# Kernel optimization log

Hardware: AMD Instinct MI355X
Metric: run time of the kernel (lower is better)

## Reference

```python
import jax, jax.numpy as jnp
import numpy as np

EPS_RMS = 1e-4   # RunningMeanStd epsilon (mean=0, var=1 at init)
LN_EPS = 1e-5    # torch LayerNorm default
NUM_HEADS = 16


def _layernorm(x, g, b):
    m = x.mean(-1, keepdims=True)
    v = ((x - m) ** 2).mean(-1, keepdims=True)
    return (x - m) / jnp.sqrt(v + LN_EPS) * g + b


def _rms_normalize(a):
    # RunningMeanStd.normalize with mean=0, var=1: clip(a / sqrt(1+eps), -5, 5)
    return jnp.clip(a / jnp.sqrt(1.0 + EPS_RMS), -5.0, 5.0)


def _sinusoidal_pe(pos, d):
    # pos [...,] -> [..., d]; matches torch code: div_term over arange(d//2)
    div = jnp.exp(jnp.arange(d // 2, dtype=jnp.float32) * (-np.log(1000.0) / d))
    ang = pos[..., None] * div                         # [..., d//2]
    pe = jnp.zeros(pos.shape + (d,), dtype=jnp.float32)
    pe = pe.at[..., 0::2].set(jnp.sin(ang))
    pe = pe.at[..., 1::2].set(jnp.cos(ang))
    return pe


def _encoder_layer(xs, mask, Wqkv, bqkv, Wo, bo, g1, be1, g2, be2, Wf1, bf1, Wf2, bf2):
    # post-LN TransformerEncoderLayer with boolean attention mask [B,S,S]
    B, S, D = xs.shape
    hd = D // NUM_HEADS
    qkv = xs @ Wqkv.T + bqkv                           # [B,S,3D]
    q, k, v = jnp.split(qkv, 3, axis=-1)
    q = q.reshape(B, S, NUM_HEADS, hd).transpose(0, 2, 1, 3)
    k = k.reshape(B, S, NUM_HEADS, hd).transpose(0, 2, 1, 3)
    v = v.reshape(B, S, NUM_HEADS, hd).transpose(0, 2, 1, 3)
    scores = jnp.einsum('bhqd,bhkd->bhqk', q, k) / jnp.sqrt(jnp.float32(hd))
    scores = jnp.where(mask[:, None, :, :], -jnp.inf, scores)
    attn = jax.nn.softmax(scores, axis=-1)
    o = jnp.einsum('bhqk,bhkd->bhqd', attn, v).transpose(0, 2, 1, 3).reshape(B, S, D)
    o = o @ Wo.T + bo
    xs = _layernorm(xs + o, g1, be1)
    ff = jax.nn.gelu(xs @ Wf1.T + bf1, approximate=False) @ Wf2.T + bf2
    xs = _layernorm(xs + ff, g2, be2)
    return xs


def reference(x, w, y, W_nail, b_nail, W_cond, b_cond, Wqkv, bqkv, Wo, bo,
              ln1_g, ln1_b, ln2_g, ln2_b, W1, b1, W2, b2, W_ham, b_ham):
    B, Lx = x.shape[0], x.shape[1]
    n_w = w.shape[1] * w.shape[2]
    L = Lx + n_w + 1                                   # total_paragraph_length
    S = L - 1
    D = W_nail.shape[0]

    w_last = w[:, -1]                                  # [B, P, 6]

    # embed_x
    t = jnp.nan_to_num(x[..., 0])
    xc = jnp.nan_to_num(x)
    xx = _rms_normalize(xc)[..., 1:] @ W_nail.T + b_nail   # [B,Lx,D]
    xx = xx + _sinusoidal_pe(t, D)
    x_mask = jnp.isnan(x[..., 0])                      # [B,Lx]

    # embed_w
    wc = jnp.nan_to_num(w)
    wn = _rms_normalize(wc).reshape(B, -1, w.shape[-1])    # [B,Lw*P,6]
    ww = wn @ W_cond.T + b_cond                        # [B,Lw*P,D]

    tgt = jnp.concatenate([xx, ww], axis=1)            # [B,S,D]

    # custom per-batch boolean mask: causal, but columns [0,Lx) follow x padding mask
    causal = jnp.triu(jnp.ones((S, S), dtype=bool), 1)
    mask = jnp.broadcast_to(causal, (B, S, S))
    mask = mask.at[:, :, :Lx].set(x_mask[:, None, :])

    # global positional encoding added only on the w-token segment
    pe_g = _sinusoidal_pe(jnp.arange(L, dtype=jnp.float32), D)  # [L,D]
    tgt = tgt.at[:, Lx:].add(pe_g[Lx:L - 1])

    for i in range(Wqkv.shape[0]):
        tgt = _encoder_layer(tgt, mask, Wqkv[i], bqkv[i], Wo[i], bo[i],
                             ln1_g[i], ln1_b[i], ln2_g[i], ln2_b[i],
                             W1[i], b1[i], W2[i], b2[i])

    y_resid_hat = (tgt[:, -1] @ W_ham.T + b_ham).reshape(B, -1, 6)
    y_resid = jax.lax.stop_gradient(y - w_last)
    loss = jnp.mean((y_resid_hat - y_resid) ** 2)
    return loss


def setup_inputs() -> dict:
    key = jax.random.key(0)
    ks = jax.random.split(key, 16)
    NL, D, FF, HAM = 4, 1024, 4096, 144
    s = 0.02
    return {
        'x': jax.random.normal(ks[0], (8, 512, 64), jnp.float32),
        'w': jax.random.normal(ks[1], (8, 16, 24, 6), jnp.float32),
        'y': jax.random.normal(ks[2], (8, 24, 6), jnp.float32),
        'W_nail': jax.random.normal(ks[3], (D, 63), jnp.float32) * s,
        'b_nail': jnp.zeros((D,), jnp.float32),
        'W_cond': jax.random.normal(ks[4], (D, 6), jnp.float32) * s,
        'b_cond': jnp.zeros((D,), jnp.float32),
        'Wqkv': jax.random.normal(ks[5], (NL, 3 * D, D), jnp.float32) * s,
        'bqkv': jnp.zeros((NL, 3 * D), jnp.float32),
        'Wo': jax.random.normal(ks[6], (NL, D, D), jnp.float32) * s,
        'bo': jnp.zeros((NL, D), jnp.float32),
        'ln1_g': jnp.ones((NL, D), jnp.float32),
        'ln1_b': jnp.zeros((NL, D), jnp.float32),
        'ln2_g': jnp.ones((NL, D), jnp.float32),
        'ln2_b': jnp.zeros((NL, D), jnp.float32),
        'W1': jax.random.normal(ks[7], (NL, FF, D), jnp.float32) * s,
        'b1': jnp.zeros((NL, FF), jnp.float32),
        'W2': jax.random.normal(ks[8], (NL, D, FF), jnp.float32) * s,
        'b2': jnp.zeros((NL, D), jnp.float32),
        'W_ham': jax.random.normal(ks[9], (HAM, D), jnp.float32) * s,
        'b_ham': jnp.zeros((HAM,), jnp.float32),
    }
```

## Files before the change

### kernel.cpp

```cpp
#include <hip/hip_runtime.h>
#include <math.h>


#define B_      8
#define LX_     512
#define NW_     384
#define S_      896
#define D_      1024
#define H_      16
#define HD_     64
#define FF_     4096
#define HAM_    144

#define RMS_SCALE 0.9999500037496876f
#define PE_C     (-6.907755278982137f / 1024.0f)

typedef __bf16 bf16x4 __attribute__((ext_vector_type(4)));
typedef __bf16 bf16x8 __attribute__((ext_vector_type(8)));
typedef float  f32x4  __attribute__((ext_vector_type(4)));

static __device__ __forceinline__ float nan0(float v) { return (v != v) ? 0.0f : v; }

static __device__ __forceinline__ void async_copy16(const __bf16* g, __bf16* l) {
    __builtin_amdgcn_global_load_lds(
        (const __attribute__((address_space(1))) void*)g,
        (__attribute__((address_space(3))) void*)l, 16, 0, 0);
}

static __device__ __forceinline__ float fast_gelu(float x) {
    float x3 = x * x * x;
    float z = 0.7978845608028654f * x + 0.035677408136300125f * x3;
    float az = fabsf(z);
    float e = __expf(2.0f * az);
    float t = 1.0f - 2.0f / (e + 1.0f);
    t = (z < 0.0f) ? -t : t;
    return 0.5f * x * (1.0f + t);
}

__global__ __launch_bounds__(256) void convert4_kernel(
        const float* __restrict__ s0, const float* __restrict__ s1,
        const float* __restrict__ s2, const float* __restrict__ s3,
        __bf16* __restrict__ d0, __bf16* __restrict__ d1,
        __bf16* __restrict__ d2, __bf16* __restrict__ d3) {
    int blk = blockIdx.x;
    const float* src; __bf16* dst; int base;
    if (blk < 3072)      { src = s0; dst = d0; base = blk; }
    else if (blk < 4096) { src = s1; dst = d1; base = blk - 3072; }
    else if (blk < 8192) { src = s2; dst = d2; base = blk - 4096; }
    else                 { src = s3; dst = d3; base = blk - 8192; }
    int i = (base * 256 + threadIdx.x) * 4;
    float4 v = *(const float4*)&src[i];
    bf16x4 o = {(__bf16)v.x, (__bf16)v.y, (__bf16)v.z, (__bf16)v.w};
    *(bf16x4*)&dst[i] = o;
}

__global__ __launch_bounds__(256) void transpose_nail_kernel(
        const float* __restrict__ W_nail, float* __restrict__ WT) {
    int i = blockIdx.x * 256 + threadIdx.x;
    int d = i & 1023, kk = i >> 10;
    WT[kk * 1024 + d] = W_nail[d * 63 + kk];
}

__global__ __launch_bounds__(256) void embed_x_kernel(
        const float* __restrict__ x, const float* __restrict__ WT,
        const float* __restrict__ b_nail, __bf16* __restrict__ tgt_bf,
        int* __restrict__ xmask) {
    int row0 = blockIdx.x * 8;
    int tid = threadIdx.x;
    __shared__ float xn[8][64];
    __shared__ float ts[8];
#pragma unroll
    for (int it = 0; it < 2; ++it) {
        int i = tid + it * 256;
        int r = i >> 6, c = i & 63;
        float vv = x[(size_t)(row0 + r) * 64 + c];
        float v0 = nan0(vv);
        xn[r][c] = fminf(fmaxf(v0 * RMS_SCALE, -5.0f), 5.0f);
        if (c == 0) { ts[r] = v0; xmask[row0 + r] = (vv != vv) ? 1 : 0; }
    }
    __syncthreads();
    int d0 = tid * 4;
    float4 bz = *(const float4*)&b_nail[d0];
    float acc[8][4];
#pragma unroll
    for (int r = 0; r < 8; ++r) {
        acc[r][0] = bz.x; acc[r][1] = bz.y; acc[r][2] = bz.z; acc[r][3] = bz.w;
    }
    for (int k = 0; k < 63; ++k) {
        float4 wv = *(const float4*)&WT[k * 1024 + d0];
#pragma unroll
        for (int r = 0; r < 8; ++r) {
            float xv = xn[r][k + 1];
            acc[r][0] += xv * wv.x; acc[r][1] += xv * wv.y;
            acc[r][2] += xv * wv.z; acc[r][3] += xv * wv.w;
        }
    }
    float div[4];
#pragma unroll
    for (int j = 0; j < 4; ++j)
        div[j] = __expf((float)((d0 + j) >> 1) * PE_C);
#pragma unroll
    for (int r = 0; r < 8; ++r) {
        int row = row0 + r;
        int b = row >> 9, i = row & 511;
        float t = ts[r];
        bf16x4 ob;
#pragma unroll
        for (int j = 0; j < 4; ++j) {
            float ang = t * div[j];
            float pe = ((d0 + j) & 1) ? __cosf(ang) : __sinf(ang);
            ob[j] = (__bf16)(acc[r][j] + pe);
        }
        *(bf16x4*)&tgt_bf[((size_t)b * S_ + i) * D_ + d0] = ob;
    }
}

__global__ __launch_bounds__(256) void embed_w_kernel(
        const float* __restrict__ w, const float* __restrict__ W_cond,
        const float* __restrict__ b_cond, __bf16* __restrict__ tgt_bf) {
    int row = blockIdx.x;
    int b = row / NW_, j = row % NW_;
    const float* wr = w + (long)row * 6;
    float wn[6];
#pragma unroll
    for (int k = 0; k < 6; ++k)
        wn[k] = fminf(fmaxf(nan0(wr[k]) * RMS_SCALE, -5.0f), 5.0f);
    int tid = threadIdx.x;
    int d0 = tid * 4;
    float pos = (float)(LX_ + j);
    bf16x4 ob;
#pragma unroll
    for (int jj = 0; jj < 4; ++jj) {
        int d = d0 + jj;
        float acc = b_cond[d];
        const float* wc = W_cond + (long)d * 6;
#pragma unroll
        for (int k = 0; k < 6; ++k) acc += wn[k] * wc[k];
        float dv = expf((float)(d >> 1) * PE_C);
        float ang = pos * dv;
        ob[jj] = (__bf16)(acc + ((d & 1) ? cosf(ang) : sinf(ang)));
    }
    *(bf16x4*)&tgt_bf[((long)b * S_ + LX_ + j) * D_ + d0] = ob;
}


#define LDA(BUF, MH) do {                                                      \
    _Pragma("unroll")                                                          \
    for (int i_ = 0; i_ < 4; ++i_) {                                           \
        const int row_ = (MH) * 128 + wr * 64 + i_ * 16 + frow;                \
        _Pragma("unroll")                                                      \
        for (int k_ = 0; k_ < 2; ++k_)                                         \
            a[i_][k_] = *(const bf16x8*)&As[BUF][row_ * 64 +                   \
                (((quad + k_ * 4) ^ sf) * 8)];                                 \
    }                                                                          \
} while (0)

#define LDB(BUF, NH) do {                                                      \
    _Pragma("unroll")                                                          \
    for (int j_ = 0; j_ < NJ; ++j_) {                                          \
        const int row_ = (BN == 256)                                           \
            ? ((NH) * 128 + j_ * 16 + wc * 32 + frow)                          \
            : ((NH) * 64 + wc * 16 + frow);                                    \
        _Pragma("unroll")                                                      \
        for (int k_ = 0; k_ < 2; ++k_)                                         \
            b[(NH) * NJ + j_][k_] = *(const bf16x8*)&Bs[BUF][row_ * 64 +       \
                (((quad + k_ * 4) ^ sf) * 8)];                                 \
    }                                                                          \
} while (0)

#define MMA(MH, NH) do {                                                       \
    _Pragma("unroll")                                                          \
    for (int i_ = 0; i_ < 4; ++i_)                                             \
        _Pragma("unroll")                                                      \
        for (int j_ = 0; j_ < NJ; ++j_)                                        \
            _Pragma("unroll")                                                  \
            for (int k_ = 0; k_ < 2; ++k_)                                     \
                acc[(MH) * 4 + i_][(NH) * NJ + j_] =                           \
                    __builtin_amdgcn_mfma_f32_16x16x32_bf16(                   \
                        b[(NH) * NJ + j_][k_], a[i_][k_],                      \
                        acc[(MH) * 4 + i_][(NH) * NJ + j_], 0, 0, 0);          \
} while (0)

#define STAGE_A(BUF, H, KT) do {                                               \
    const __bf16* g_ = Ag + (size_t)((H) * 128) * K + ((size_t)(KT) << 6);     \
    async_copy16(g_, &As[BUF][((H) * 128) * 64 + dst8]);                       \
    async_copy16(g_ + ((size_t)K << 6), &As[BUF][((H) * 128 + 64) * 64 + dst8]); \
} while (0)

#define STAGE_B(BUF, H, KT) do {                                               \
    if constexpr (BN == 256) {                                                 \
        const __bf16* g_ = Wg + (size_t)((H) * 128) * K + ((size_t)(KT) << 6); \
        async_copy16(g_, &Bs[BUF][((H) * 128) * 64 + dst8]);                   \
        async_copy16(g_ + ((size_t)K << 6),                                    \
                     &Bs[BUF][((H) * 128 + 64) * 64 + dst8]);                  \
    } else {                                                                   \
        const __bf16* g_ = Wg + (size_t)((H) * 64) * K + ((size_t)(KT) << 6);  \
        async_copy16(g_, &Bs[BUF][((H) * 64) * 64 + dst8]);                    \
    }                                                                          \
} while (0)

#define PHASE_SYNC() do {                                                      \
    __builtin_amdgcn_sched_barrier(0);                                         \
    __builtin_amdgcn_s_barrier();                                              \
    asm volatile("s_waitcnt lgkmcnt(0)" ::: "memory");                         \
    __builtin_amdgcn_sched_barrier(0);                                         \
} while (0)

#define PHASE_END() do {                                                       \
    __builtin_amdgcn_sched_barrier(0);                                         \
    __builtin_amdgcn_s_barrier();                                              \
} while (0)

#define VM_MAIN do {                                                           \
    if constexpr (BN == 256) { asm volatile("s_waitcnt vmcnt(6)" ::: "memory"); } \
    else                     { asm volatile("s_waitcnt vmcnt(4)" ::: "memory"); } \
} while (0)
#define VM_ZERO asm volatile("s_waitcnt vmcnt(0)" ::: "memory")
#define VM_NONE ((void)0)

#define GTILE(S1, S2, VMOP) do {                                               \
    const int bf_ = t & 1;                                                     \
                          \
    LDA(bf_, 0); LDB(bf_, 0);                                                  \
    if (S1) STAGE_A(bf_ ^ 1, 1, t + 1);                                        \
    PHASE_SYNC();                                                              \
    __builtin_amdgcn_s_setprio(1); MMA(0, 0); __builtin_amdgcn_s_setprio(0);   \
    PHASE_END();                                                               \
                    \
    LDB(bf_, 1);                                                               \
    if (S2) STAGE_B(bf_, 0, t + 2);                                            \
    PHASE_SYNC();                                                              \
    __builtin_amdgcn_s_setprio(1); MMA(0, 1); __builtin_amdgcn_s_setprio(0);   \
    PHASE_END();                                                               \
                                     \
    LDA(bf_, 1);                                                               \
    if (S2) STAGE_A(bf_, 0, t + 2);                                            \
    PHASE_SYNC();                                                              \
    __builtin_amdgcn_s_setprio(1); MMA(1, 0); __builtin_amdgcn_s_setprio(0);   \
    PHASE_END();                                                               \
            \
    if (S2) STAGE_B(bf_, 1, t + 2);                                            \
    VMOP;                                                                      \
    PHASE_SYNC();                                                              \
    __builtin_amdgcn_s_setprio(1); MMA(1, 1); __builtin_amdgcn_s_setprio(0);   \
    PHASE_END();                                                               \
} while (0)

template <int BN, int MODE>
__global__ __launch_bounds__(512, 2) void gemm8p(
        const __bf16* __restrict__ A, const __bf16* __restrict__ W,
        const float* __restrict__ bias,
        __bf16* __restrict__ Cb,
        __bf16* __restrict__ Cq, __bf16* __restrict__ Ck, __bf16* __restrict__ Cv,
        int M, int N, int K) {
    constexpr int NI = BN / 64;
    constexpr int NJ = NI / 2;
    static_assert(BN == 256 || BN == 128, "BN");
    __shared__ __attribute__((aligned(16))) __bf16 As[2][256 * 64];
    __shared__ __attribute__((aligned(16))) __bf16 Bs[2][BN * 64];

    const int tid = threadIdx.x;
    const int wave = tid >> 6, lane = tid & 63;
    const int wr = wave >> 2, wc = wave & 3;
    const int frow = lane & 15, quad = lane >> 4;
    const int sf = frow & 7;
    const int m0 = blockIdx.y * 256, n0 = blockIdx.x * BN;

    const int sr = tid >> 3;
    const int scol = ((tid & 7) ^ (sr & 7)) * 8;
    const __bf16* Ag = A + (size_t)(m0 + sr) * K + scol;
    const __bf16* Wg = W + (size_t)(n0 + sr) * K + scol;
    const int dst8 = tid * 8;

    f32x4 acc[8][NI];
#pragma unroll
    for (int i = 0; i < 8; ++i)
#pragma unroll
        for (int j = 0; j < NI; ++j) acc[i][j] = 0.0f;
    bf16x8 a[4][2];
    bf16x8 b[NI][2];

    const int NT = K >> 6;

    STAGE_B(0, 0, 0); STAGE_A(0, 0, 0); STAGE_B(0, 1, 0); STAGE_A(0, 1, 0);
    STAGE_B(1, 0, 1); STAGE_A(1, 0, 1); STAGE_B(1, 1, 1);
    VM_MAIN;
    __builtin_amdgcn_s_barrier();

    int t = 0;
    for (; t < NT - 2; ++t) { GTILE(1, 1, VM_MAIN); }
    GTILE(1, 0, VM_ZERO);
    ++t;
    GTILE(0, 0, VM_NONE);

#pragma unroll
    for (int ni = 0; ni < NI; ++ni) {
        int cg0;
        if constexpr (BN == 256)
            cg0 = n0 + (ni >> 1) * 128 + (ni & 1) * 16 + wc * 32 + quad * 4;
        else
            cg0 = n0 + ni * 64 + wc * 16 + quad * 4;
        float4 bv = *(const float4*)&bias[cg0];
        float bz[4] = {bv.x, bv.y, bv.z, bv.w};
#pragma unroll
        for (int mi = 0; mi < 8; ++mi) {
            int rg = m0 + (mi >> 2) * 128 + wr * 64 + (mi & 3) * 16 + frow;
            float vv[4];
#pragma unroll
            for (int r = 0; r < 4; ++r) {
                float v = acc[mi][ni][r] + bz[r];
                if (MODE == 1) v = fast_gelu(v);
                vv[r] = v;
            }
            bf16x4 o = {(__bf16)vv[0], (__bf16)vv[1], (__bf16)vv[2], (__bf16)vv[3]};
            if (MODE == 2) {
                int which = cg0 >> 10;
                int h = (cg0 & 1023) >> 6;
                int e = cg0 & 63;
                int bb = rg / S_, s = rg % S_;
                __bf16* dstp = (which == 0) ? Cq : (which == 1) ? Ck : Cv;
                *(bf16x4*)&dstp[(((size_t)bb * H_ + h) * S_ + s) * HD_ + e] = o;
            } else {
                *(bf16x4*)&Cb[(size_t)rg * N + cg0] = o;
            }
        }
    }
}

__global__ __launch_bounds__(256) void attn_mfma(
        const __bf16* __restrict__ q, const __bf16* __restrict__ k,
        const __bf16* __restrict__ v, const int* __restrict__ xmask,
        __bf16* __restrict__ ctx) {
    __shared__ __bf16 Ks[64][72];
    __shared__ __bf16 Vt[64][66];
    __shared__ __bf16 Ps[4][16][72];
    __shared__ float mb[LX_];
    int tid = threadIdx.x;
    int wave = tid >> 6, lane = tid & 63;
    int frow = lane & 15, quad = lane >> 4;
    int blk = blockIdx.x;
    int qt = blk % 14;
    int bh = blk / 14;
    int b = bh >> 4, h = bh & 15;
    int q0 = qt * 64;
    int q0w = q0 + wave * 16;
    size_t base = (size_t)bh * S_ * HD_;

    for (int i = tid; i < LX_; i += 256)
        mb[i] = xmask[(b << 9) + i] ? -INFINITY : 0.0f;

    const __bf16* qrow = q + base + (size_t)(q0w + frow) * HD_ + quad * 8;
    bf16x8 aq0 = *(const bf16x8*)qrow;
    bf16x8 aq1 = *(const bf16x8*)(qrow + 32);

    f32x4 o[4];
#pragma unroll
    for (int dt = 0; dt < 4; ++dt) o[dt] = 0.0f;
    float mrow[4] = {-INFINITY, -INFINITY, -INFINITY, -INFINITY};
    float lrow[4] = {0.0f, 0.0f, 0.0f, 0.0f};

    int kend = (q0 >= LX_) ? (q0 + 64) : LX_;

    int sr = tid >> 2;
    int sc = (tid & 3) * 8;
    const __bf16* kg = k + base + (size_t)sr * HD_ + sc;
    const __bf16* vg = v + base + (size_t)sr * HD_ + sc;

    for (int k0 = 0; k0 < kend; k0 += 64) {
        {
            size_t off = (size_t)k0 * HD_;
            bf16x8 k0v = *(const bf16x8*)(kg + off);
            bf16x8 k1v = *(const bf16x8*)(kg + off + 32);
            *(bf16x8*)&Ks[sr][sc] = k0v;
            *(bf16x8*)&Ks[sr][sc + 32] = k1v;
            bf16x8 v0v = *(const bf16x8*)(vg + off);
            bf16x8 v1v = *(const bf16x8*)(vg + off + 32);
#pragma unroll
            for (int j = 0; j < 8; ++j) {
                Vt[sc + j][sr] = v0v[j];
                Vt[sc + 32 + j][sr] = v1v[j];
            }
        }
        __syncthreads();

        f32x4 scr[4];
#pragma unroll
        for (int nt = 0; nt < 4; ++nt) {
            bf16x8 bk0 = *(const bf16x8*)&Ks[nt * 16 + frow][quad * 8];
            bf16x8 bk1 = *(const bf16x8*)&Ks[nt * 16 + frow][32 + quad * 8];
            f32x4 z = 0.0f;
            z = __builtin_amdgcn_mfma_f32_16x16x32_bf16(aq0, bk0, z, 0, 0, 0);
            z = __builtin_amdgcn_mfma_f32_16x16x32_bf16(aq1, bk1, z, 0, 0, 0);
            scr[nt] = z;
        }

        float tmax[4] = {-INFINITY, -INFINITY, -INFINITY, -INFINITY};
#pragma unroll
        for (int nt = 0; nt < 4; ++nt) {
            int kj = k0 + nt * 16 + frow;
            float bias = (kj < LX_) ? mb[kj] : 0.0f;
#pragma unroll
            for (int r = 0; r < 4; ++r) {
                float s = scr[nt][r] * 0.125f + bias;
                if (kj >= LX_ && kj > q0w + quad * 4 + r) s = -INFINITY;
                scr[nt][r] = s;
                tmax[r] = fmaxf(tmax[r], s);
            }
        }
#pragma unroll
        for (int off = 1; off < 16; off <<= 1)
#pragma unroll
            for (int r = 0; r < 4; ++r)
                tmax[r] = fmaxf(tmax[r], __shfl_xor(tmax[r], off, 64));

        float alpha[4], rsum[4];
#pragma unroll
        for (int r = 0; r < 4; ++r) {
            float nm = fmaxf(mrow[r], tmax[r]);
            alpha[r] = (nm == -INFINITY) ? 1.0f : __expf(mrow[r] - nm);
            mrow[r] = nm;
            rsum[r] = 0.0f;
        }
#pragma unroll
        for (int nt = 0; nt < 4; ++nt) {
#pragma unroll
            for (int r = 0; r < 4; ++r) {
                float s = scr[nt][r];
                float p = (s == -INFINITY) ? 0.0f : __expf(s - mrow[r]);
                rsum[r] += p;
                Ps[wave][quad * 4 + r][nt * 16 + frow] = (__bf16)p;
            }
        }
#pragma unroll
        for (int off = 1; off < 16; off <<= 1)
#pragma unroll
            for (int r = 0; r < 4; ++r)
                rsum[r] += __shfl_xor(rsum[r], off, 64);
#pragma unroll
        for (int r = 0; r < 4; ++r)
            lrow[r] = lrow[r] * alpha[r] + rsum[r];
#pragma unroll
        for (int dt = 0; dt < 4; ++dt)
#pragma unroll
            for (int r = 0; r < 4; ++r)
                o[dt][r] *= alpha[r];

        bf16x8 ap0 = *(const bf16x8*)&Ps[wave][frow][quad * 8];
        bf16x8 ap1 = *(const bf16x8*)&Ps[wave][frow][32 + quad * 8];
#pragma unroll
        for (int dt = 0; dt < 4; ++dt) {
            bf16x8 bv0 = *(const bf16x8*)&Vt[dt * 16 + frow][quad * 8];
            bf16x8 bv1 = *(const bf16x8*)&Vt[dt * 16 + frow][32 + quad * 8];
            o[dt] = __builtin_amdgcn_mfma_f32_16x16x32_bf16(ap0, bv0, o[dt], 0, 0, 0);
            o[dt] = __builtin_amdgcn_mfma_f32_16x16x32_bf16(ap1, bv1, o[dt], 0, 0, 0);
        }
        __syncthreads();
    }

#pragma unroll
    for (int r = 0; r < 4; ++r) {
        float inv = (lrow[r] > 0.0f) ? 1.0f / lrow[r] : 0.0f;
        int qg = q0w + quad * 4 + r;
        size_t ob = ((size_t)b * S_ + qg) * D_ + h * HD_;
#pragma unroll
        for (int dt = 0; dt < 4; ++dt)
            ctx[ob + dt * 16 + frow] = (__bf16)(o[dt][r] * inv);
    }
}

__global__ __launch_bounds__(256) void add_ln_kernel(
        __bf16* __restrict__ xs_bf, const __bf16* __restrict__ o,
        const float* __restrict__ g, const float* __restrict__ bb) {
    long row = blockIdx.x;
    __bf16* xr = xs_bf + row * D_;
    const __bf16* orr = o + row * D_;
    int tid = threadIdx.x;
    bf16x4 a4 = *(const bf16x4*)&xr[tid * 4];
    bf16x4 b4v = *(const bf16x4*)&orr[tid * 4];
    float vv[4];
#pragma unroll
    for (int j = 0; j < 4; ++j) vv[j] = (float)a4[j] + (float)b4v[j];
    float s = vv[0] + vv[1] + vv[2] + vv[3];
    __shared__ float red[4];
    __shared__ float stat;
#pragma unroll
    for (int off = 32; off; off >>= 1) s += __shfl_down(s, off, 64);
    if ((tid & 63) == 0) red[tid >> 6] = s;
    __syncthreads();
    if (tid == 0) stat = (red[0] + red[1] + red[2] + red[3]) * (1.0f / 1024.0f);
    __syncthreads();
    float mean = stat;
    float d[4];
    float s2 = 0.0f;
#pragma unroll
    for (int j = 0; j < 4; ++j) { d[j] = vv[j] - mean; s2 += d[j] * d[j]; }
    __syncthreads();
#pragma unroll
    for (int off = 32; off; off >>= 1) s2 += __shfl_down(s2, off, 64);
    if ((tid & 63) == 0) red[tid >> 6] = s2;
    __syncthreads();
    if (tid == 0) stat = (red[0] + red[1] + red[2] + red[3]) * (1.0f / 1024.0f);
    __syncthreads();
    float inv = 1.0f / sqrtf(stat + 1e-5f);
    float4 gg = *(const float4*)&g[tid * 4];
    float4 bv = *(const float4*)&bb[tid * 4];
    float g4[4] = {gg.x, gg.y, gg.z, gg.w};
    float b4[4] = {bv.x, bv.y, bv.z, bv.w};
    bf16x4 ob;
#pragma unroll
    for (int j = 0; j < 4; ++j) ob[j] = (__bf16)(d[j] * inv * g4[j] + b4[j]);
    *(bf16x4*)&xr[tid * 4] = ob;
}

__global__ __launch_bounds__(256) void head_kernel(
        const __bf16* __restrict__ tgt_bf, const float* __restrict__ W_ham,
        const float* __restrict__ b_ham, float* __restrict__ out) {
    int b = blockIdx.x;
    int tid = threadIdx.x;
    __shared__ float xr[D_];
    const __bf16* row = tgt_bf + ((long)b * S_ + (S_ - 1)) * D_;
    for (int i = tid; i < D_; i += 256) xr[i] = (float)row[i];
    __syncthreads();
    for (int n = tid; n < HAM_; n += 256) {
        float acc = b_ham[n];
        const float* wr = W_ham + (long)n * D_;
        for (int kk = 0; kk < D_; ++kk) acc += xr[kk] * wr[kk];
        out[b * HAM_ + n] = acc;
    }
}

__global__ __launch_bounds__(256) void loss_kernel(
        const float* __restrict__ head_out, const float* __restrict__ y,
        const float* __restrict__ w, float* __restrict__ out) {
    int tid = threadIdx.x;
    float acc = 0.0f;
    for (int i = tid; i < B_ * HAM_; i += 256) {
        int b = i / HAM_, r = i % HAM_;
        float w_last = w[((long)b * 16 + 15) * HAM_ + r];
        float resid = y[i] - w_last;
        float dd = head_out[i] - resid;
        acc += dd * dd;
    }
    __shared__ float red[4];
#pragma unroll
    for (int off = 32; off; off >>= 1) acc += __shfl_down(acc, off, 64);
    if ((tid & 63) == 0) red[tid >> 6] = acc;
    __syncthreads();
    if (tid == 0)
        out[0] = (red[0] + red[1] + red[2] + red[3]) * (1.0f / (B_ * HAM_));
}

extern "C" void kernel_launch(void* const* d_in, const int* in_sizes, int n_in,
                              void* d_out, int out_size, void* d_ws, size_t ws_size,
                              hipStream_t stream) {
    const float* x      = (const float*)d_in[0];
    const float* w      = (const float*)d_in[1];
    const float* y      = (const float*)d_in[2];
    const float* W_nail = (const float*)d_in[3];
    const float* b_nail = (const float*)d_in[4];
    const float* W_cond = (const float*)d_in[5];
    const float* b_cond = (const float*)d_in[6];
    const float* Wqkv   = (const float*)d_in[7];
    const float* bqkv   = (const float*)d_in[8];
    const float* Wo     = (const float*)d_in[9];
    const float* bo     = (const float*)d_in[10];
    const float* ln1_g  = (const float*)d_in[11];
    const float* ln1_b  = (const float*)d_in[12];
    const float* ln2_g  = (const float*)d_in[13];
    const float* ln2_b  = (const float*)d_in[14];
    const float* W1     = (const float*)d_in[15];
    const float* b1     = (const float*)d_in[16];
    const float* W2     = (const float*)d_in[17];
    const float* b2     = (const float*)d_in[18];
    const float* W_ham  = (const float*)d_in[19];
    const float* b_ham  = (const float*)d_in[20];

    float* ws = (float*)d_ws;
    const long SEG = (long)B_ * S_ * D_;
    float*  W_nailT = ws;
    __bf16* tmp_bf = (__bf16*)(ws + SEG);
    __bf16* tgt_bf = (__bf16*)(ws + 2 * SEG);
    __bf16* ctx_bf = (__bf16*)(ws + 2 * SEG + SEG / 2);
    __bf16* qb     = (__bf16*)(ws + 3 * SEG);
    __bf16* kb     = (__bf16*)(ws + 3 * SEG + SEG / 2);
    __bf16* vb     = (__bf16*)(ws + 4 * SEG);
    __bf16* ffh_bf = (__bf16*)(ws + 2 * SEG + SEG / 2);
    __bf16* wbf    = (__bf16*)(ws + 4 * SEG + SEG / 2);
    int*    xmask    = (int*)(ws + 4 * SEG + SEG / 2 + 6291456);
    float*  head_out = ws + 4 * SEG + SEG / 2 + 6291456 + 4096;

    __bf16* wqkv_bf = wbf;
    __bf16* wo_bf   = wbf + 3145728;
    __bf16* w1_bf   = wbf + 4194304;
    __bf16* w2_bf   = wbf + 8388608;

    const int M = B_ * S_;

    transpose_nail_kernel<<<252, 256, 0, stream>>>(W_nail, W_nailT);
    embed_x_kernel<<<B_ * LX_ / 8, 256, 0, stream>>>(x, W_nailT, b_nail, tgt_bf, xmask);
    embed_w_kernel<<<B_ * NW_, 256, 0, stream>>>(w, W_cond, b_cond, tgt_bf);

    for (int L = 0; L < 4; ++L) {
        const int NQ = 3 * D_ * D_, NO = D_ * D_, N1 = FF_ * D_, N2 = D_ * FF_;
        convert4_kernel<<<12288, 256, 0, stream>>>(
            Wqkv + (size_t)L * NQ, Wo + (size_t)L * NO,
            W1 + (size_t)L * N1, W2 + (size_t)L * N2,
            wqkv_bf, wo_bf, w1_bf, w2_bf);

        gemm8p<256, 2><<<dim3(3 * D_ / 256, M / 256), 512, 0, stream>>>(
            tgt_bf, wqkv_bf, bqkv + (size_t)L * 3 * D_,
            nullptr, qb, kb, vb, M, 3 * D_, D_);
        attn_mfma<<<B_ * H_ * (S_ / 64), 256, 0, stream>>>(qb, kb, vb, xmask, ctx_bf);
        gemm8p<128, 0><<<dim3(D_ / 128, M / 256), 512, 0, stream>>>(
            ctx_bf, wo_bf, bo + (size_t)L * D_,
            tmp_bf, nullptr, nullptr, nullptr, M, D_, D_);
        add_ln_kernel<<<M, 256, 0, stream>>>(tgt_bf, tmp_bf,
            ln1_g + (size_t)L * D_, ln1_b + (size_t)L * D_);
        gemm8p<256, 1><<<dim3(FF_ / 256, M / 256), 512, 0, stream>>>(
            tgt_bf, w1_bf, b1 + (size_t)L * FF_,
            ffh_bf, nullptr, nullptr, nullptr, M, FF_, D_);
        gemm8p<128, 0><<<dim3(D_ / 128, M / 256), 512, 0, stream>>>(
            ffh_bf, w2_bf, b2 + (size_t)L * D_,
            tmp_bf, nullptr, nullptr, nullptr, M, D_, FF_);
        add_ln_kernel<<<M, 256, 0, stream>>>(tgt_bf, tmp_bf,
            ln2_g + (size_t)L * D_, ln2_b + (size_t)L * D_);
    }

    head_kernel<<<B_, 256, 0, stream>>>(tgt_bf, W_ham, b_ham, head_out);
    loss_kernel<<<1, 256, 0, stream>>>(head_out, y, w, (float*)d_out);
}
```

Before: 1.874 ms.

## Store V transposed from QKV GEMM and double-buffer attention K/V with async LDS loads

The QKV GEMM epilogue now writes V in a [b,h,d,s] transposed layout, so attention can stream K and V tiles straight into XOR-swizzled LDS with async global-to-LDS copies. The tiles are double-buffered, with the next one prefetched while the current one is computed, and MFMA sections get raised priority. The out-projection GEMM switches to a simpler 128x128 kernel with 256 threads. Attention blocks are also remapped so that the blocks for one (b,h) land on the same XCD. The trade-off is that the transposed V writes become scalar scattered stores in the QKV epilogue.

```diff
diff --git a/kernel.cpp b/kernel.cpp
--- a/kernel.cpp
+++ b/kernel.cpp
@@ -220,25 +220,21 @@
 
 #define GTILE(S1, S2, VMOP) do {                                               \
     const int bf_ = t & 1;                                                     \
-                          \
     LDA(bf_, 0); LDB(bf_, 0);                                                  \
     if (S1) STAGE_A(bf_ ^ 1, 1, t + 1);                                        \
     PHASE_SYNC();                                                              \
     __builtin_amdgcn_s_setprio(1); MMA(0, 0); __builtin_amdgcn_s_setprio(0);   \
     PHASE_END();                                                               \
-                    \
     LDB(bf_, 1);                                                               \
     if (S2) STAGE_B(bf_, 0, t + 2);                                            \
     PHASE_SYNC();                                                              \
     __builtin_amdgcn_s_setprio(1); MMA(0, 1); __builtin_amdgcn_s_setprio(0);   \
     PHASE_END();                                                               \
-                                     \
     LDA(bf_, 1);                                                               \
     if (S2) STAGE_A(bf_, 0, t + 2);                                            \
     PHASE_SYNC();                                                              \
     __builtin_amdgcn_s_setprio(1); MMA(1, 0); __builtin_amdgcn_s_setprio(0);   \
     PHASE_END();                                                               \
-            \
     if (S2) STAGE_B(bf_, 1, t + 2);                                            \
     VMOP;                                                                      \
     PHASE_SYNC();                                                              \
@@ -312,39 +308,137 @@
                 if (MODE == 1) v = fast_gelu(v);
                 vv[r] = v;
             }
-            bf16x4 o = {(__bf16)vv[0], (__bf16)vv[1], (__bf16)vv[2], (__bf16)vv[3]};
             if (MODE == 2) {
                 int which = cg0 >> 10;
                 int h = (cg0 & 1023) >> 6;
                 int e = cg0 & 63;
                 int bb = rg / S_, s = rg % S_;
-                __bf16* dstp = (which == 0) ? Cq : (which == 1) ? Ck : Cv;
-                *(bf16x4*)&dstp[(((size_t)bb * H_ + h) * S_ + s) * HD_ + e] = o;
+                if (which == 2) {
+                    size_t vb = ((size_t)bb * H_ + h) * HD_ + e;
+#pragma unroll
+                    for (int r = 0; r < 4; ++r)
+                        Cv[(vb + r) * S_ + s] = (__bf16)vv[r];
+                } else {
+                    bf16x4 o = {(__bf16)vv[0], (__bf16)vv[1], (__bf16)vv[2], (__bf16)vv[3]};
+                    __bf16* dstp = (which == 0) ? Cq : Ck;
+                    *(bf16x4*)&dstp[(((size_t)bb * H_ + h) * S_ + s) * HD_ + e] = o;
+                }
             } else {
+                bf16x4 o = {(__bf16)vv[0], (__bf16)vv[1], (__bf16)vv[2], (__bf16)vv[3]};
                 *(bf16x4*)&Cb[(size_t)rg * N + cg0] = o;
             }
         }
     }
 }
 
+template <int MODE>
+__global__ __launch_bounds__(256) void gemm_mfma(
+        const __bf16* __restrict__ A, const __bf16* __restrict__ W,
+        const float* __restrict__ bias,
+        __bf16* __restrict__ Cb,
+        int M, int N, int K) {
+    __shared__ __bf16 As[128 * 64];
+    __shared__ __bf16 Bs[128 * 64];
+    int tid = threadIdx.x;
+    int wave = tid >> 6, lane = tid & 63;
+    int m0 = blockIdx.y * 128, n0 = blockIdx.x * 128;
+    int wm = (wave >> 1) * 64, wn = (wave & 1) * 64;
+
+    int srow = wave * 32 + (lane >> 3);
+    int scol = ((lane & 7) ^ (lane >> 3)) * 8;
+    const __bf16* Ag = A + (size_t)(m0 + srow) * K + scol;
+    const __bf16* Wg = W + (size_t)(n0 + srow) * K + scol;
+    __bf16* Al = &As[wave * 2048];
+    __bf16* Bl = &Bs[wave * 2048];
+
+    f32x4 acc[4][4];
+#pragma unroll
+    for (int i = 0; i < 4; ++i)
+#pragma unroll
+        for (int j = 0; j < 4; ++j) acc[i][j] = 0.0f;
+
+    int frow = lane & 15;
+    int quad = lane >> 4;
+    int sf = frow & 7;
+
+    for (int k0 = 0; k0 < K; k0 += 64) {
+        size_t off = (size_t)k0;
+        async_copy16(Ag + off,                  Al);
+        async_copy16(Ag + off + (size_t)8 * K,  Al + 512);
+        async_copy16(Ag + off + (size_t)16 * K, Al + 1024);
+        async_copy16(Ag + off + (size_t)24 * K, Al + 1536);
+        async_copy16(Wg + off,                  Bl);
+        async_copy16(Wg + off + (size_t)8 * K,  Bl + 512);
+        async_copy16(Wg + off + (size_t)16 * K, Bl + 1024);
+        async_copy16(Wg + off + (size_t)24 * K, Bl + 1536);
+        __syncthreads();
+#pragma unroll
+        for (int ks = 0; ks < 2; ++ks) {
+            int slot = ((quad + ks * 4) ^ sf) * 8;
+            bf16x8 a[4], b[4];
+#pragma unroll
+            for (int mi = 0; mi < 4; ++mi)
+                a[mi] = *(const bf16x8*)&As[(wm + mi * 16 + frow) * 64 + slot];
+#pragma unroll
+            for (int ni = 0; ni < 4; ++ni)
+                b[ni] = *(const bf16x8*)&Bs[(wn + ni * 16 + frow) * 64 + slot];
+#pragma unroll
+            for (int mi = 0; mi < 4; ++mi)
+#pragma unroll
+                for (int ni = 0; ni < 4; ++ni)
+                    acc[mi][ni] = __builtin_amdgcn_mfma_f32_16x16x32_bf16(
+                        b[ni], a[mi], acc[mi][ni], 0, 0, 0);
+        }
+        __syncthreads();
+    }
+
+    int mrow_l = lane & 15;
+    int nq = (lane >> 4) * 4;
+#pragma unroll
+    for (int ni = 0; ni < 4; ++ni) {
+        int cg0 = n0 + wn + ni * 16 + nq;
+        float4 bv = *(const float4*)&bias[cg0];
+        float bz[4] = {bv.x, bv.y, bv.z, bv.w};
+#pragma unroll
+        for (int mi = 0; mi < 4; ++mi) {
+            int rg = m0 + wm + mi * 16 + mrow_l;
+            float vv[4];
+#pragma unroll
+            for (int r = 0; r < 4; ++r) {
+                float v = acc[mi][ni][r] + bz[r];
+                if (MODE == 1) v = fast_gelu(v);
+                vv[r] = v;
+            }
+            bf16x4 o = {(__bf16)vv[0], (__bf16)vv[1], (__bf16)vv[2], (__bf16)vv[3]};
+            *(bf16x4*)&Cb[(size_t)rg * N + cg0] = o;
+        }
+    }
+}
+
 __global__ __launch_bounds__(256) void attn_mfma(
         const __bf16* __restrict__ q, const __bf16* __restrict__ k,
-        const __bf16* __restrict__ v, const int* __restrict__ xmask,
+        const __bf16* __restrict__ vt, const int* __restrict__ xmask,
         __bf16* __restrict__ ctx) {
-    __shared__ __bf16 Ks[64][72];
-    __shared__ __bf16 Vt[64][66];
-    __shared__ __bf16 Ps[4][16][72];
+    __shared__ __attribute__((aligned(16))) __bf16 Ks[2][64 * 64];
+    __shared__ __attribute__((aligned(16))) __bf16 Vs[2][64 * 64];
+    __shared__ __attribute__((aligned(16))) __bf16 Ps[4][16 * 64];
     __shared__ float mb[LX_];
     int tid = threadIdx.x;
     int wave = tid >> 6, lane = tid & 63;
     int frow = lane & 15, quad = lane >> 4;
+    int f7 = frow & 7, f3 = frow >> 3;
+    int sl0 = (quad ^ f7) * 8;
+    int sl1 = ((quad + 4) ^ f7) * 8;
+
     int blk = blockIdx.x;
-    int qt = blk % 14;
-    int bh = blk / 14;
+    int xcd = blk & 7, slot = blk >> 3;
+    int bh = xcd * 16 + slot / 14;
+    int qt = slot % 14;
     int b = bh >> 4, h = bh & 15;
     int q0 = qt * 64;
     int q0w = q0 + wave * 16;
     size_t base = (size_t)bh * S_ * HD_;
+    size_t vbase = (size_t)bh * HD_ * S_;
 
     for (int i = tid; i < LX_; i += 256)
         mb[i] = xmask[(b << 9) + i] ? -INFINITY : 0.0f;
@@ -360,39 +454,50 @@
     float lrow[4] = {0.0f, 0.0f, 0.0f, 0.0f};
 
     int kend = (q0 >= LX_) ? (q0 + 64) : LX_;
-
-    int sr = tid >> 2;
-    int sc = (tid & 3) * 8;
-    const __bf16* kg = k + base + (size_t)sr * HD_ + sc;
-    const __bf16* vg = v + base + (size_t)sr * HD_ + sc;
-
-    for (int k0 = 0; k0 < kend; k0 += 64) {
-        {
-            size_t off = (size_t)k0 * HD_;
-            bf16x8 k0v = *(const bf16x8*)(kg + off);
-            bf16x8 k1v = *(const bf16x8*)(kg + off + 32);
-            *(bf16x8*)&Ks[sr][sc] = k0v;
-            *(bf16x8*)&Ks[sr][sc + 32] = k1v;
-            bf16x8 v0v = *(const bf16x8*)(vg + off);
-            bf16x8 v1v = *(const bf16x8*)(vg + off + 32);
-#pragma unroll
-            for (int j = 0; j < 8; ++j) {
-                Vt[sc + j][sr] = v0v[j];
-                Vt[sc + 32 + j][sr] = v1v[j];
-            }
-        }
-        __syncthreads();
+    int NT = kend >> 6;
+
+    int srow = tid >> 3;
+    int kcol = ((tid & 7) ^ (srow & 7)) * 8;
+    const __bf16* kg = k + base + (size_t)srow * HD_ + kcol;
+    const __bf16* vg = vt + vbase + (size_t)srow * S_ + kcol;
+
+#define ASTAGE(BUF, K0) do {                                                   \
+    const __bf16* kg_ = kg + (size_t)(K0) * HD_;                               \
+    async_copy16(kg_,                  &Ks[BUF][tid * 8]);                     \
+    async_copy16(kg_ + 32 * HD_,       &Ks[BUF][2048 + tid * 8]);              \
+    const __bf16* vg_ = vg + (K0);                                             \
+    async_copy16(vg_,                  &Vs[BUF][tid * 8]);                     \
+    async_copy16(vg_ + 32 * S_,        &Vs[BUF][2048 + tid * 8]);              \
+} while (0)
+
+    ASTAGE(0, 0);
+    __syncthreads();
+
+    for (int t = 0; t < NT; ++t) {
+        int buf = t & 1;
+        int k0 = t << 6;
+        if (t + 1 < NT) {
+            ASTAGE(buf ^ 1, k0 + 64);
+            asm volatile("s_waitcnt vmcnt(4)" ::: "memory");
+        } else {
+            asm volatile("s_waitcnt vmcnt(0)" ::: "memory");
+        }
+        __builtin_amdgcn_s_barrier();
+        __builtin_amdgcn_sched_barrier(0);
 
         f32x4 scr[4];
+        __builtin_amdgcn_s_setprio(1);
 #pragma unroll
         for (int nt = 0; nt < 4; ++nt) {
-            bf16x8 bk0 = *(const bf16x8*)&Ks[nt * 16 + frow][quad * 8];
-            bf16x8 bk1 = *(const bf16x8*)&Ks[nt * 16 + frow][32 + quad * 8];
+            int row = (nt * 16 + frow) * 64;
+            bf16x8 bk0 = *(const bf16x8*)&Ks[buf][row + sl0];
+            bf16x8 bk1 = *(const bf16x8*)&Ks[buf][row + sl1];
             f32x4 z = 0.0f;
             z = __builtin_amdgcn_mfma_f32_16x16x32_bf16(aq0, bk0, z, 0, 0, 0);
             z = __builtin_amdgcn_mfma_f32_16x16x32_bf16(aq1, bk1, z, 0, 0, 0);
             scr[nt] = z;
         }
+        __builtin_amdgcn_s_setprio(0);
 
         float tmax[4] = {-INFINITY, -INFINITY, -INFINITY, -INFINITY};
 #pragma unroll
@@ -428,7 +533,9 @@
                 float s = scr[nt][r];
                 float p = (s == -INFINITY) ? 0.0f : __expf(s - mrow[r]);
                 rsum[r] += p;
-                Ps[wave][quad * 4 + r][nt * 16 + frow] = (__bf16)p;
+                int ql = quad * 4 + r;
+                int pslot = ((nt * 2 + f3) ^ (ql & 7)) * 8 + f7;
+                Ps[wave][ql * 64 + pslot] = (__bf16)p;
             }
         }
 #pragma unroll
@@ -445,17 +552,22 @@
             for (int r = 0; r < 4; ++r)
                 o[dt][r] *= alpha[r];
 
-        bf16x8 ap0 = *(const bf16x8*)&Ps[wave][frow][quad * 8];
-        bf16x8 ap1 = *(const bf16x8*)&Ps[wave][frow][32 + quad * 8];
+        bf16x8 ap0 = *(const bf16x8*)&Ps[wave][frow * 64 + sl0];
+        bf16x8 ap1 = *(const bf16x8*)&Ps[wave][frow * 64 + sl1];
+        __builtin_amdgcn_s_setprio(1);
 #pragma unroll
         for (int dt = 0; dt < 4; ++dt) {
-            bf16x8 bv0 = *(const bf16x8*)&Vt[dt * 16 + frow][quad * 8];
-            bf16x8 bv1 = *(const bf16x8*)&Vt[dt * 16 + frow][32 + quad * 8];
+            int row = (dt * 16 + frow) * 64;
+            bf16x8 bv0 = *(const bf16x8*)&Vs[buf][row + sl0];
+            bf16x8 bv1 = *(const bf16x8*)&Vs[buf][row + sl1];
             o[dt] = __builtin_amdgcn_mfma_f32_16x16x32_bf16(ap0, bv0, o[dt], 0, 0, 0);
             o[dt] = __builtin_amdgcn_mfma_f32_16x16x32_bf16(ap1, bv1, o[dt], 0, 0, 0);
         }
-        __syncthreads();
-    }
+        __builtin_amdgcn_s_setprio(0);
+        __builtin_amdgcn_sched_barrier(0);
+        __builtin_amdgcn_s_barrier();
+    }
+#undef ASTAGE
 
 #pragma unroll
     for (int r = 0; r < 4; ++r) {
@@ -611,9 +723,9 @@
             tgt_bf, wqkv_bf, bqkv + (size_t)L * 3 * D_,
             nullptr, qb, kb, vb, M, 3 * D_, D_);
         attn_mfma<<<B_ * H_ * (S_ / 64), 256, 0, stream>>>(qb, kb, vb, xmask, ctx_bf);
-        gemm8p<128, 0><<<dim3(D_ / 128, M / 256), 512, 0, stream>>>(
+        gemm_mfma<0><<<dim3(D_ / 128, M / 128), 256, 0, stream>>>(
             ctx_bf, wo_bf, bo + (size_t)L * D_,
-            tmp_bf, nullptr, nullptr, nullptr, M, D_, D_);
+            tmp_bf, M, D_, D_);
         add_ln_kernel<<<M, 256, 0, stream>>>(tgt_bf, tmp_bf,
             ln1_g + (size_t)L * D_, ln1_b + (size_t)L * D_);
         gemm8p<256, 1><<<dim3(FF_ / 256, M / 256), 512, 0, stream>>>(
```

Measured after the change: 1.798 ms. -4.0%, faster.
